# Optimization experiments

Measured on AMD Instinct MI355X. Metric: run time of the kernel, lower is better.

## Reference

```python
import jax, jax.numpy as jnp
import numpy as np

DIM = 1024
N_HEAD = 16
HEAD_DIM = DIM // N_HEAD
SCALE = HEAD_DIM ** (-0.5)


def setup_inputs() -> dict:
    key = jax.random.key(0)
    ks = jax.random.split(key, 5)
    x = jax.random.normal(ks[0], (2, 2048, DIM), dtype=jnp.float32)
    # Linear params (torch nn.Linear stores weight as [out, in]; we keep [in, out])
    wqkv = jax.random.normal(ks[1], (DIM, 3 * DIM), dtype=jnp.float32) / np.sqrt(DIM)
    bqkv = jax.random.normal(ks[2], (3 * DIM,), dtype=jnp.float32) * 0.01
    wo = jax.random.normal(ks[3], (DIM, DIM), dtype=jnp.float32) / np.sqrt(DIM)
    bo = jax.random.normal(ks[4], (DIM,), dtype=jnp.float32) * 0.01
    return {"x": x, "wqkv": wqkv, "bqkv": bqkv, "wo": wo, "bo": bo}


def reference(x, wqkv, bqkv, wo, bo):
    b, s, _ = x.shape
    qkv = x @ wqkv + bqkv                      # [b, s, 3*dim]
    q, k, v = jnp.split(qkv, 3, axis=-1)
    # [b, s, h, d] -> [b, h, s, d]
    def heads(t):
        return t.reshape(b, s, N_HEAD, HEAD_DIM).transpose(0, 2, 1, 3)
    q, k, v = heads(q) * SCALE, heads(k), heads(v)
    attn = jnp.einsum('bhqd,bhkd->bhqk', q, k)  # [b, h, s, s]
    attn = jax.nn.softmax(attn, axis=-1)
    out = jnp.einsum('bhqk,bhkd->bhqd', attn, v)
    out = out.transpose(0, 2, 1, 3).reshape(b, s, DIM)
    return out @ wo + bo
```

## Files before the change

kernel.cpp:

```cpp
#include <hip/hip_runtime.h>
#include <hip/hip_bf16.h>

#define DIM   1024
#define NHEAD 16
#define HDIM  64
#define BATCH 2
#define SEQ   2048
#define TOK   (BATCH*SEQ)
#define QSCALE 0.1803368801111204f

typedef unsigned short u16;
typedef __attribute__((ext_vector_type(8))) _Float16 h16x8;
typedef __attribute__((ext_vector_type(2))) __fp16 fp16x2;
typedef __attribute__((ext_vector_type(4))) float f32x4;
typedef __attribute__((ext_vector_type(16))) float f32x16;
typedef __attribute__((ext_vector_type(2))) int i32x2;

__device__ __forceinline__ u16 f2h(float f) {
    union { _Float16 h; u16 u; } v; v.h = (_Float16)f;
    return v.u;
}
__device__ __forceinline__ unsigned pack2h(float a, float b) {
    return (unsigned)f2h(a) | ((unsigned)f2h(b) << 16);
}
__device__ __forceinline__ unsigned pkrtz(float a, float b) {
    union { fp16x2 h; unsigned u; } v;
    v.h = __builtin_amdgcn_cvt_pkrtz(a, b);
    return v.u;
}
__device__ __forceinline__ f32x16 zero16() {
    f32x16 v;
#pragma unroll
    for (int i = 0; i < 16; ++i) v[i] = 0.f;
    return v;
}

typedef __attribute__((address_space(3))) void lds_void;
typedef const __attribute__((address_space(1))) void gbl_void;
__device__ __forceinline__ void gload_lds16(const void* g, void* l) {
    __builtin_amdgcn_global_load_lds((gbl_void*)g, (lds_void*)l, 16, 0, 0);
}

__global__ __launch_bounds__(256)
void fused_cvt(const float* __restrict__ x,    u16* __restrict__ xh,
               const float* __restrict__ wqkv, u16* __restrict__ wqT,
               const float* __restrict__ wo,   u16* __restrict__ woT) {
    __shared__ float t[32][33];
    const int bid = blockIdx.x;
    if (bid < 4096) {
        int i = bid * 256 + threadIdx.x;
        float4 v = ((const float4*)x)[i];
        ((uint2*)xh)[i] = make_uint2(pack2h(v.x, v.y), pack2h(v.z, v.w));
        return;
    }
    const float* in; u16* outT; int K, N, tb;
    if (bid < 7168) { in = wqkv; outT = wqT; K = 1024; N = 3072; tb = bid - 4096; }
    else            { in = wo;   outT = woT; K = 1024; N = 1024; tb = bid - 7168; }
    const int nbx = N / 32;
    const int n0 = (tb % nbx) * 32, k0 = (tb / nbx) * 32;
    const int tx = threadIdx.x & 31, ty = threadIdx.x >> 5;
#pragma unroll
    for (int i = 0; i < 4; ++i)
        t[ty + i * 8][tx] = in[(size_t)(k0 + ty + i * 8) * N + n0 + tx];
    __syncthreads();
#pragma unroll
    for (int i = 0; i < 4; ++i)
        outT[(size_t)(n0 + ty + i * 8) * K + k0 + tx] = f2h(t[tx][ty + i * 8]);
}

__global__ __launch_bounds__(256)
void gemm_qkv(const u16* __restrict__ Ag, const u16* __restrict__ Bg,
              const float* __restrict__ bias, u16* __restrict__ Qh,
              u16* __restrict__ Kh, u16* __restrict__ Vh, int K, int N) {
    __shared__ u16 As[128 * 64];
    __shared__ u16 Bs[128 * 64];

    const int tid  = threadIdx.x;
    const int lane = tid & 63;
    const int w    = tid >> 6;
    const int c    = lane & 15;
    const int quad = lane >> 4;
    const int wm   = (w & 1) * 64;
    const int wn   = (w >> 1) * 64;
    const int row0 = blockIdx.y * 128;
    const int col0 = blockIdx.x * 128;
    const int sw   = c & 7;

    f32x4 acc[4][4];
#pragma unroll
    for (int m = 0; m < 4; ++m)
#pragma unroll
        for (int n = 0; n < 4; ++n) acc[m][n] = (f32x4){0.f, 0.f, 0.f, 0.f};

    for (int k0 = 0; k0 < K; k0 += 64) {
        __syncthreads();
#pragma unroll
        for (int i = 0; i < 4; ++i) {
            int idx = tid + i * 256;
            int r = idx >> 3, p = idx & 7;
            int g = p ^ (r & 7);
            gload_lds16(Ag + (size_t)(row0 + r) * K + k0 + g * 8, &As[idx * 8]);
            gload_lds16(Bg + (size_t)(col0 + r) * K + k0 + g * 8, &Bs[idx * 8]);
        }
        __syncthreads();

        h16x8 af[4][2];
#pragma unroll
        for (int m = 0; m < 4; ++m)
#pragma unroll
            for (int kh = 0; kh < 2; ++kh)
                af[m][kh] = *(const h16x8*)&As[(wm + m * 16 + c) * 64 +
                                              ((kh * 4 + quad) ^ sw) * 8];
#pragma unroll
        for (int kh = 0; kh < 2; ++kh)
#pragma unroll
            for (int n = 0; n < 4; ++n) {
                h16x8 bf = *(const h16x8*)&Bs[(wn + n * 16 + c) * 64 +
                                              ((kh * 4 + quad) ^ sw) * 8];
#pragma unroll
                for (int m = 0; m < 4; ++m)
                    acc[m][n] = __builtin_amdgcn_mfma_f32_16x16x32_f16(
                        af[m][kh], bf, acc[m][n], 0, 0, 0);
            }
    }

#pragma unroll
    for (int n = 0; n < 4; ++n) {
        const int col = col0 + wn + n * 16 + c;
        const float bv = bias[col];
        const int h = (col >> 6) & 15, d = col & 63;
#pragma unroll
        for (int m = 0; m < 4; ++m) {
            const int rbase = row0 + wm + m * 16 + quad * 4;
            const int b = rbase >> 11, s0 = rbase & (SEQ - 1);
            const int bh = (b << 4) + h;
            if (col0 < DIM) {
#pragma unroll
                for (int r = 0; r < 4; ++r)
                    Qh[((size_t)bh * SEQ + s0 + r) * 64 + d] =
                        f2h((acc[m][n][r] + bv) * QSCALE);
            } else if (col0 < 2 * DIM) {
#pragma unroll
                for (int r = 0; r < 4; ++r)
                    Kh[((size_t)bh * SEQ + s0 + r) * 64 + d] =
                        f2h(acc[m][n][r] + bv);
            } else {
                uint2 pv = make_uint2(pack2h(acc[m][n][0] + bv, acc[m][n][1] + bv),
                                      pack2h(acc[m][n][2] + bv, acc[m][n][3] + bv));
                *(uint2*)&Vh[((size_t)bh * 64 + d) * SEQ + s0] = pv;
            }
        }
    }
}

__global__ __launch_bounds__(256)
void gemm_out(const u16* __restrict__ Ag, const u16* __restrict__ Bg,
              const float* __restrict__ bias, float* __restrict__ Cout,
              int M, int N, int K) {
    __shared__ u16 As[128 * 64];
    __shared__ u16 Bs[128 * 64];

    const int tid  = threadIdx.x;
    const int lane = tid & 63;
    const int w    = tid >> 6;
    const int c    = lane & 15;
    const int quad = lane >> 4;
    const int wm   = (w & 1) * 64;
    const int wn   = (w >> 1) * 64;
    const int row0 = blockIdx.y * 128;
    const int col0 = blockIdx.x * 128;
    const int sw   = c & 7;

    f32x4 acc[4][4];
#pragma unroll
    for (int m = 0; m < 4; ++m)
#pragma unroll
        for (int n = 0; n < 4; ++n) acc[m][n] = (f32x4){0.f, 0.f, 0.f, 0.f};

    for (int k0 = 0; k0 < K; k0 += 64) {
        __syncthreads();
#pragma unroll
        for (int i = 0; i < 4; ++i) {
            int idx = tid + i * 256;
            int r = idx >> 3, p = idx & 7;
            int g = p ^ (r & 7);
            gload_lds16(Ag + (size_t)(row0 + r) * K + k0 + g * 8, &As[idx * 8]);
            gload_lds16(Bg + (size_t)(col0 + r) * K + k0 + g * 8, &Bs[idx * 8]);
        }
        __syncthreads();

        h16x8 af[4][2];
#pragma unroll
        for (int m = 0; m < 4; ++m)
#pragma unroll
            for (int kh = 0; kh < 2; ++kh)
                af[m][kh] = *(const h16x8*)&As[(wm + m * 16 + c) * 64 +
                                              ((kh * 4 + quad) ^ sw) * 8];
#pragma unroll
        for (int kh = 0; kh < 2; ++kh)
#pragma unroll
            for (int n = 0; n < 4; ++n) {
                h16x8 bf = *(const h16x8*)&Bs[(wn + n * 16 + c) * 64 +
                                              ((kh * 4 + quad) ^ sw) * 8];
#pragma unroll
                for (int m = 0; m < 4; ++m)
                    acc[m][n] = __builtin_amdgcn_mfma_f32_16x16x32_f16(
                        af[m][kh], bf, acc[m][n], 0, 0, 0);
            }
    }

#pragma unroll
    for (int n = 0; n < 4; ++n) {
        const int col = col0 + wn + n * 16 + c;
        const float bv = bias[col];
#pragma unroll
        for (int m = 0; m < 4; ++m) {
            const int rbase = row0 + wm + m * 16 + quad * 4;
#pragma unroll
            for (int r = 0; r < 4; ++r)
                Cout[(size_t)(rbase + r) * N + col] = acc[m][n][r] + bv;
        }
    }
}

__global__ __launch_bounds__(256, 2)
void flash_attn14(const u16* __restrict__ Qg, const u16* __restrict__ Kg,
                  const u16* __restrict__ Vg, u16* __restrict__ aout) {
    __shared__ u16 KV[2][64 * 128];
    __shared__ float lc[256];

    u16* Ks = KV[0];
    u16* Vt = KV[1];

    const int tid  = threadIdx.x;
    const int lane = tid & 63;
    const int w    = tid >> 6;
    const int wq   = w & 1;
    const int wk   = w >> 1;
    const int n32  = lane & 31;
    const int q5   = lane >> 5;
    const int bh   = blockIdx.y;
    const int q0   = blockIdx.x * 128;

    const u16* Qb = Qg + (size_t)bh * SEQ * 64;
    const u16* Kb = Kg + (size_t)bh * SEQ * 64;
    const u16* Vb = Vg + (size_t)bh * 64 * SEQ;

    const int qrowA = wq * 64 + n32;
    const int qrowB = qrowA + 32;
    const int sw    = n32 & 7;

    h16x8 qbA[4], qbB[4];
    {
        const u16* qa  = Qb + (size_t)(q0 + qrowA) * 64;
        const u16* qb_ = Qb + (size_t)(q0 + qrowB) * 64;
#pragma unroll
        for (int s = 0; s < 4; ++s) {
            qbA[s] = *(const h16x8*)&qa[(s * 2 + q5) * 8];
            qbB[s] = *(const h16x8*)&qb_[(s * 2 + q5) * 8];
        }
    }

    float lA = 0.f, lB = 0.f;
    f32x16 oA[2] = {zero16(), zero16()};
    f32x16 oB[2] = {zero16(), zero16()};

    for (int kt = 0; kt < SEQ / 128; ++kt) {
        const int k1 = kt * 128;

        if (kt) __syncthreads();

#pragma unroll
        for (int i = 0; i < 4; ++i) {
            int idx = tid + i * 256;
            int rk = idx >> 3, pk = idx & 7, gk = pk ^ (rk & 7);
            gload_lds16(Kb + (size_t)(k1 + rk) * 64 + gk * 8, &Ks[idx * 8]);
            int rv = idx >> 4, cv = idx & 15, gv = cv ^ (rv & 7);
            gload_lds16(Vb + (size_t)rv * SEQ + k1 + gv * 8, &Vt[idx * 8]);
        }
        __syncthreads();

        unsigned xwA[8][2], xwB[8][2];
#pragma unroll
        for (int sub = 0; sub < 2; ++sub) {
            const int kr = wk * 64 + sub * 32 + n32;
            f32x16 saA = zero16(), saB = zero16();
            __builtin_amdgcn_s_setprio(1);
#pragma unroll
            for (int s = 0; s < 4; ++s) {
                h16x8 ak = *(const h16x8*)&Ks[kr * 64 +
                                              (((s * 2 + q5) ^ sw) * 8)];
                saA = __builtin_amdgcn_mfma_f32_32x32x16_f16(ak, qbA[s], saA, 0, 0, 0);
                saB = __builtin_amdgcn_mfma_f32_32x32x16_f16(ak, qbB[s], saB, 0, 0, 0);
            }
            __builtin_amdgcn_s_setprio(0);
#pragma unroll
            for (int rr = 0; rr < 4; ++rr) {
                float a0 = __builtin_amdgcn_exp2f(saA[4 * rr + 0]);
                float a1 = __builtin_amdgcn_exp2f(saA[4 * rr + 1]);
                float a2 = __builtin_amdgcn_exp2f(saA[4 * rr + 2]);
                float a3 = __builtin_amdgcn_exp2f(saA[4 * rr + 3]);
                lA += (a0 + a1) + (a2 + a3);
                xwA[sub * 4 + rr][0] = pkrtz(a0, a1);
                xwA[sub * 4 + rr][1] = pkrtz(a2, a3);
                float b0 = __builtin_amdgcn_exp2f(saB[4 * rr + 0]);
                float b1 = __builtin_amdgcn_exp2f(saB[4 * rr + 1]);
                float b2 = __builtin_amdgcn_exp2f(saB[4 * rr + 2]);
                float b3 = __builtin_amdgcn_exp2f(saB[4 * rr + 3]);
                lB += (b0 + b1) + (b2 + b3);
                xwB[sub * 4 + rr][0] = pkrtz(b0, b1);
                xwB[sub * 4 + rr][1] = pkrtz(b2, b3);
            }
        }

        h16x8 bpA[4], bpB[4];
#pragma unroll
        for (int s = 0; s < 4; ++s) {
            i32x2 ra = __builtin_amdgcn_permlane32_swap(
                (int)xwA[2 * s][0], (int)xwA[2 * s + 1][0], false, false);
            i32x2 rb = __builtin_amdgcn_permlane32_swap(
                (int)xwA[2 * s][1], (int)xwA[2 * s + 1][1], false, false);
            union { int u[4]; h16x8 h; } fa;
            fa.u[0] = ra[0]; fa.u[1] = rb[0]; fa.u[2] = ra[1]; fa.u[3] = rb[1];
            bpA[s] = fa.h;
            i32x2 rc = __builtin_amdgcn_permlane32_swap(
                (int)xwB[2 * s][0], (int)xwB[2 * s + 1][0], false, false);
            i32x2 rd = __builtin_amdgcn_permlane32_swap(
                (int)xwB[2 * s][1], (int)xwB[2 * s + 1][1], false, false);
            union { int u[4]; h16x8 h; } fb;
            fb.u[0] = rc[0]; fb.u[1] = rd[0]; fb.u[2] = rc[1]; fb.u[3] = rd[1];
            bpB[s] = fb.h;
        }

        __builtin_amdgcn_s_setprio(1);
#pragma unroll
        for (int dt = 0; dt < 2; ++dt) {
            const int dr = dt * 32 + n32;
#pragma unroll
            for (int s = 0; s < 4; ++s) {
                h16x8 av = *(const h16x8*)&Vt[dr * 128 +
                                              ((wk * 8 + ((s * 2 + q5) ^ sw)) * 8)];
                oA[dt] = __builtin_amdgcn_mfma_f32_32x32x16_f16(av, bpA[s], oA[dt], 0, 0, 0);
                oB[dt] = __builtin_amdgcn_mfma_f32_32x32x16_f16(av, bpB[s], oB[dt], 0, 0, 0);
            }
        }
        __builtin_amdgcn_s_setprio(0);
    }
    __syncthreads();

    lA += __shfl_xor(lA, 32, 64);
    lB += __shfl_xor(lB, 32, 64);

    float* oc = (float*)KV;
    const int rowA = (wq * 2 + 0) * 64 + lane;
    const int rowB = (wq * 2 + 1) * 64 + lane;
    if (wk == 1) {
#pragma unroll
        for (int dt = 0; dt < 2; ++dt)
#pragma unroll
            for (int i = 0; i < 16; ++i) {
                oc[rowA * 32 + ((dt * 16 + i + lane) & 31)] = oA[dt][i];
                oc[rowB * 32 + ((dt * 16 + i + lane) & 31)] = oB[dt][i];
            }
        lc[rowA] = lA;
        lc[rowB] = lB;
    }
    __syncthreads();
    if (wk == 1) return;
    lA += lc[rowA];
    lB += lc[rowB];
#pragma unroll
    for (int dt = 0; dt < 2; ++dt)
#pragma unroll
        for (int i = 0; i < 16; ++i) {
            oA[dt][i] += oc[rowA * 32 + ((dt * 16 + i + lane) & 31)];
            oB[dt][i] += oc[rowB * 32 + ((dt * 16 + i + lane) & 31)];
        }

    const float invA = 1.f / lA, invB = 1.f / lB;
    const int b = bh >> 4, h = bh & 15;
    const size_t roA = (size_t)(b * SEQ + q0 + qrowA) * DIM + h * HDIM;
    const size_t roB = (size_t)(b * SEQ + q0 + qrowB) * DIM + h * HDIM;
#pragma unroll
    for (int dt = 0; dt < 2; ++dt) {
#pragma unroll
        for (int rq = 0; rq < 4; ++rq) {
            const int d = dt * 32 + 8 * rq + 4 * q5;
            *(uint2*)&aout[roA + d] = make_uint2(
                pkrtz(oA[dt][4 * rq + 0] * invA, oA[dt][4 * rq + 1] * invA),
                pkrtz(oA[dt][4 * rq + 2] * invA, oA[dt][4 * rq + 3] * invA));
            *(uint2*)&aout[roB + d] = make_uint2(
                pkrtz(oB[dt][4 * rq + 0] * invB, oB[dt][4 * rq + 1] * invB),
                pkrtz(oB[dt][4 * rq + 2] * invB, oB[dt][4 * rq + 3] * invB));
        }
    }
}

extern "C" void kernel_launch(void* const* d_in, const int* in_sizes, int n_in,
                              void* d_out, int out_size, void* d_ws, size_t ws_size,
                              hipStream_t stream) {
    (void)in_sizes; (void)n_in; (void)out_size; (void)ws_size;
    const float* x    = (const float*)d_in[0];
    const float* wqkv = (const float*)d_in[1];
    const float* bqkv = (const float*)d_in[2];
    const float* wo   = (const float*)d_in[3];
    const float* bo   = (const float*)d_in[4];
    float* out = (float*)d_out;

    const size_t HB = (size_t)BATCH * NHEAD * SEQ * HDIM;
    u16* Qh  = (u16*)d_ws;
    u16* Kh  = Qh + HB;
    u16* Vh  = Kh + HB;
    u16* ao  = Vh + HB;
    u16* wqT = ao + (size_t)TOK * DIM;
    u16* woT = wqT + (size_t)3 * DIM * DIM;
    u16* xh  = woT + (size_t)DIM * DIM;

    fused_cvt<<<8192, 256, 0, stream>>>(x, xh, wqkv, wqT, wo, woT);
    gemm_qkv<<<dim3(3 * DIM / 128, TOK / 128), 256, 0, stream>>>(
        xh, wqT, bqkv, Qh, Kh, Vh, DIM, 3 * DIM);
    flash_attn14<<<dim3(SEQ / 128, BATCH * NHEAD), 256, 0, stream>>>(
        Qh, Kh, Vh, ao);
    gemm_out<<<dim3(DIM / 128, TOK / 128), 256, 0, stream>>>(
        ao, woT, bo, out, TOK, DIM, DIM);
}
```

Measured before the change: 189.2 us.

## Split attention over two KV halves with a separate combine kernel

```diff
diff --git a/kernel.cpp b/kernel.cpp
--- a/kernel.cpp
+++ b/kernel.cpp
@@ -7,6 +7,7 @@
 #define BATCH 2
 #define SEQ   2048
 #define TOK   (BATCH*SEQ)
+#define ROWS  (BATCH*NHEAD*SEQ)
 #define QSCALE 0.1803368801111204f
 
 typedef unsigned short u16;
@@ -224,8 +225,9 @@
 }
 
 __global__ __launch_bounds__(256, 2)
-void flash_attn14(const u16* __restrict__ Qg, const u16* __restrict__ Kg,
-                  const u16* __restrict__ Vg, u16* __restrict__ aout) {
+void flash_attn15(const u16* __restrict__ Qg, const u16* __restrict__ Kg,
+                  const u16* __restrict__ Vg, u16* __restrict__ Op,
+                  float* __restrict__ lp) {
     __shared__ u16 KV[2][64 * 128];
     __shared__ float lc[256];
 
@@ -240,6 +242,7 @@
     const int n32  = lane & 31;
     const int q5   = lane >> 5;
     const int bh   = blockIdx.y;
+    const int ks   = blockIdx.z;
     const int q0   = blockIdx.x * 128;
 
     const u16* Qb = Qg + (size_t)bh * SEQ * 64;
@@ -265,10 +268,10 @@
     f32x16 oA[2] = {zero16(), zero16()};
     f32x16 oB[2] = {zero16(), zero16()};
 
-    for (int kt = 0; kt < SEQ / 128; ++kt) {
-        const int k1 = kt * 128;
-
-        if (kt) __syncthreads();
+    for (int it = 0; it < 8; ++it) {
+        const int k1 = (ks * 8 + it) * 128;
+
+        if (it) __syncthreads();
 
 #pragma unroll
         for (int i = 0; i < 4; ++i) {
@@ -377,23 +380,46 @@
             oB[dt][i] += oc[rowB * 32 + ((dt * 16 + i + lane) & 31)];
         }
 
-    const float invA = 1.f / lA, invB = 1.f / lB;
-    const int b = bh >> 4, h = bh & 15;
-    const size_t roA = (size_t)(b * SEQ + q0 + qrowA) * DIM + h * HDIM;
-    const size_t roB = (size_t)(b * SEQ + q0 + qrowB) * DIM + h * HDIM;
+    const size_t prow = (size_t)(ks * (BATCH * NHEAD) + bh) * SEQ + q0;
+    if (q5 == 0) {
+        lp[prow + qrowA] = lA;
+        lp[prow + qrowB] = lB;
+    }
+    u16* opA = Op + (prow + qrowA) * 64;
+    u16* opB = Op + (prow + qrowB) * 64;
 #pragma unroll
     for (int dt = 0; dt < 2; ++dt) {
 #pragma unroll
         for (int rq = 0; rq < 4; ++rq) {
             const int d = dt * 32 + 8 * rq + 4 * q5;
-            *(uint2*)&aout[roA + d] = make_uint2(
-                pkrtz(oA[dt][4 * rq + 0] * invA, oA[dt][4 * rq + 1] * invA),
-                pkrtz(oA[dt][4 * rq + 2] * invA, oA[dt][4 * rq + 3] * invA));
-            *(uint2*)&aout[roB + d] = make_uint2(
-                pkrtz(oB[dt][4 * rq + 0] * invB, oB[dt][4 * rq + 1] * invB),
-                pkrtz(oB[dt][4 * rq + 2] * invB, oB[dt][4 * rq + 3] * invB));
-        }
-    }
+            *(uint2*)&opA[d] = make_uint2(
+                pkrtz(oA[dt][4 * rq + 0], oA[dt][4 * rq + 1]),
+                pkrtz(oA[dt][4 * rq + 2], oA[dt][4 * rq + 3]));
+            *(uint2*)&opB[d] = make_uint2(
+                pkrtz(oB[dt][4 * rq + 0], oB[dt][4 * rq + 1]),
+                pkrtz(oB[dt][4 * rq + 2], oB[dt][4 * rq + 3]));
+        }
+    }
+}
+
+__global__ __launch_bounds__(256)
+void attn_combine(const u16* __restrict__ Op, const float* __restrict__ lp,
+                  u16* __restrict__ ao) {
+    const int t   = blockIdx.x * 256 + threadIdx.x;
+    const int row = t >> 3;
+    const int d0  = (t & 7) * 8;
+    const float inv = 1.f / (lp[row] + lp[ROWS + row]);
+    union { uint4 u; _Float16 h[8]; } a, b;
+    a.u = *(const uint4*)&Op[(size_t)row * 64 + d0];
+    b.u = *(const uint4*)&Op[((size_t)ROWS + row) * 64 + d0];
+    float s[8];
+#pragma unroll
+    for (int j = 0; j < 8; ++j) s[j] = ((float)a.h[j] + (float)b.h[j]) * inv;
+    uint4 o = make_uint4(pkrtz(s[0], s[1]), pkrtz(s[2], s[3]),
+                         pkrtz(s[4], s[5]), pkrtz(s[6], s[7]));
+    const int bh = row >> 11, q = row & (SEQ - 1);
+    const int bb = bh >> 4, h = bh & 15;
+    *(uint4*)&ao[(size_t)(bb * SEQ + q) * DIM + h * HDIM + d0] = o;
 }
 
 extern "C" void kernel_launch(void* const* d_in, const int* in_sizes, int n_in,
@@ -416,11 +442,15 @@
     u16* woT = wqT + (size_t)3 * DIM * DIM;
     u16* xh  = woT + (size_t)DIM * DIM;
 
+    u16*   Opart = (u16*)d_out;
+    float* lpart = (float*)xh;
+
     fused_cvt<<<8192, 256, 0, stream>>>(x, xh, wqkv, wqT, wo, woT);
     gemm_qkv<<<dim3(3 * DIM / 128, TOK / 128), 256, 0, stream>>>(
         xh, wqT, bqkv, Qh, Kh, Vh, DIM, 3 * DIM);
-    flash_attn14<<<dim3(SEQ / 128, BATCH * NHEAD), 256, 0, stream>>>(
-        Qh, Kh, Vh, ao);
+    flash_attn15<<<dim3(SEQ / 128, BATCH * NHEAD, 2), 256, 0, stream>>>(
+        Qh, Kh, Vh, Opart, lpart);
+    attn_combine<<<ROWS * 8 / 256, 256, 0, stream>>>(Opart, lpart, ao);
     gemm_out<<<dim3(DIM / 128, TOK / 128), 256, 0, stream>>>(
         ao, woT, bo, out, TOK, DIM, DIM);
 }
```

New measurement: 190.7 us. Within noise of the previous version (+0.8%).
